# Optimization experiments

Hardware: AMD Instinct MI355X
Metric: run time of the kernel (lower is better)

## Reference

```python
import jax, jax.numpy as jnp
import numpy as np

EMBED_DIM = 1024
NUM_HEADS = 16
HEAD_DIM = EMBED_DIM // NUM_HEADS
BSZ = 4
SEQ = 1500


def setup_inputs() -> dict:
    key = jax.random.key(0)
    ks = jax.random.split(key, 8)
    s = 0.02
    return {
        "hidden_states": jax.random.normal(ks[0], (BSZ, SEQ, EMBED_DIM), jnp.float32),
        "Wq": jax.random.normal(ks[1], (EMBED_DIM, EMBED_DIM), jnp.float32) * s,
        "bq": jax.random.normal(ks[2], (EMBED_DIM,), jnp.float32) * s,
        "Wk": jax.random.normal(ks[3], (EMBED_DIM, EMBED_DIM), jnp.float32) * s,
        "Wv": jax.random.normal(ks[4], (EMBED_DIM, EMBED_DIM), jnp.float32) * s,
        "bv": jax.random.normal(ks[5], (EMBED_DIM,), jnp.float32) * s,
        "Wo": jax.random.normal(ks[6], (EMBED_DIM, EMBED_DIM), jnp.float32) * s,
        "bo": jax.random.normal(ks[7], (EMBED_DIM,), jnp.float32) * s,
    }


def reference(hidden_states, Wq, bq, Wk, Wv, bv, Wo, bo):
    b, t, e = hidden_states.shape
    h, d = NUM_HEADS, HEAD_DIM
    scaling = d ** -0.5

    def shape(x):  # [b, t, e] -> [b, h, t, d]
        return x.reshape(b, t, h, d).transpose(0, 2, 1, 3)

    # q_proj (with bias) then scale applied to the full projected output,
    # matching the original (scale multiplies q_proj output incl. bias).
    q = shape((hidden_states @ Wq.T + bq) * scaling)
    k = shape(hidden_states @ Wk.T)            # k_proj has no bias in Whisper
    v = shape(hidden_states @ Wv.T + bv)

    # naive materialized attention scores: [b, h, t, t]
    attn_weights = jnp.einsum("bhqd,bhkd->bhqk", q, k)
    attn_probs = jax.nn.softmax(attn_weights, axis=-1)
    attn_output = jnp.einsum("bhqk,bhkd->bhqd", attn_probs, v)

    # [b, h, t, d] -> [b, t, e]
    attn_output = attn_output.transpose(0, 2, 1, 3).reshape(b, t, e)
    return attn_output @ Wo.T + bo
```

## Files before the change

### kernel.cpp

```cpp
#include <hip/hip_runtime.h>
#include <math.h>

#define E 1024
#define NH 16
#define HD 64
#define BSZ_ 4
#define SEQ_ 1500
#define M_ (BSZ_ * SEQ_)
#define SZE ((size_t)M_ * (size_t)E)
#define QSC (0.125f * 1.44269504f)

#define QA_OFF  0u
#define XB_OFF  6144000u
#define WB_OFF  12288000u
#define WOB_OFF 15433728u
#define WS_NEED_BYTES ((size_t)(16482304u) * 2u)

typedef __attribute__((ext_vector_type(8))) short short8v;
typedef __attribute__((ext_vector_type(4))) float f32x4;
typedef __attribute__((ext_vector_type(16))) float f32x16;
typedef __attribute__((ext_vector_type(4))) unsigned short ushort4v;

__device__ __forceinline__ unsigned short f2bf(float f) {
    union { float f; unsigned int i; } c; c.f = f;
    return (unsigned short)((c.i + 0x7FFFu + ((c.i >> 16) & 1u)) >> 16);
}
__device__ __forceinline__ unsigned int cvt_pk_bf16(float a, float b) {
    unsigned int r;
    asm("v_cvt_pk_bf16_f32 %0, %1, %2" : "=v"(r) : "v"(a), "v"(b));
    return r;
}

__device__ __forceinline__ int swz(int row, int col) {
    return (row << 6) + ((((col >> 3) ^ row) & 7) << 3) + (col & 7);
}
__device__ __forceinline__ int swzf(int r, int d) {
    int row = r >> 1;
    int cs = ((r & 1) << 3) | (d >> 3);
    return row * 128 + ((cs ^ (row & 15)) << 3) + (d & 7);
}

__device__ __forceinline__ short8v pack8(const float* x) {
    union { unsigned int u[4]; short8v v; } r;
    r.u[0] = cvt_pk_bf16(x[0], x[1]);
    r.u[1] = cvt_pk_bf16(x[2], x[3]);
    r.u[2] = cvt_pk_bf16(x[4], x[5]);
    r.u[3] = cvt_pk_bf16(x[6], x[7]);
    return r.v;
}

__device__ __forceinline__ void gload16(const unsigned short* g,
                                        unsigned short* l) {
    __builtin_amdgcn_global_load_lds(
        (const __attribute__((address_space(1))) unsigned int*)(g),
        (__attribute__((address_space(3))) unsigned int*)(l), 16, 0, 0);
}


__global__ __launch_bounds__(256) void cvt_kernel(
    const float* __restrict__ X,  const float* __restrict__ Wk,
    const float* __restrict__ Wv, const float* __restrict__ Wq,
    const float* __restrict__ Wo, unsigned short* __restrict__ ws)
{
    size_t w = ((size_t)blockIdx.x * 256 + threadIdx.x) * 8;
    const float* s; unsigned short* d; float sc = 1.0f;
    if (w < 6144000u)      { s = X  + w;             d = ws + XB_OFF + w; }
    else if (w < 7192576u) { s = Wk + (w - 6144000u); d = ws + WB_OFF + (w - 6144000u); }
    else if (w < 8241152u) { s = Wv + (w - 7192576u); d = ws + WB_OFF + 1048576u + (w - 7192576u); }
    else if (w < 9289728u) { s = Wq + (w - 8241152u); d = ws + WB_OFF + 2097152u + (w - 8241152u); sc = QSC; }
    else                   { s = Wo + (w - 9289728u); d = ws + WOB_OFF + (w - 9289728u); }
    float t[8];
    *(float4*)t = *(const float4*)s;
    *(float4*)(t + 4) = *(const float4*)(s + 4);
#pragma unroll
    for (int i = 0; i < 8; ++i) t[i] *= sc;
    *(short8v*)d = pack8(t);
}

__device__ __forceinline__ void gemm128b(
    const unsigned short* __restrict__ Arow,
    const unsigned short* __restrict__ Brow,
    unsigned short* As, unsigned short* Bs, int tid, f32x4 acc[4][4])
{
    const int lane = tid & 63, wid = tid >> 6;
    const int wm = tid >> 7, wn = (tid >> 6) & 1;
    for (int k0 = 0; k0 < E; k0 += 64) {
#pragma unroll
        for (int i = 0; i < 4; ++i) {
            int row = wid * 32 + i * 8 + (lane >> 3);
            int sl = (lane & 7) ^ (row & 7);
            unsigned short* lbase = As + (wid * 32 + i * 8) * 64;
            gload16(Arow + (size_t)row * E + k0 + sl * 8, lbase);
            unsigned short* lbase2 = Bs + (wid * 32 + i * 8) * 64;
            gload16(Brow + (size_t)row * E + k0 + sl * 8, lbase2);
        }
        __syncthreads();
#pragma unroll
        for (int kk = 0; kk < 64; kk += 32) {
            short8v afr[4], bfr[4];
#pragma unroll
            for (int m = 0; m < 4; ++m)
                afr[m] = *(const short8v*)(As + swz(wm * 64 + m * 16 + (lane & 15),
                                                    kk + (lane >> 4) * 8));
#pragma unroll
            for (int n = 0; n < 4; ++n)
                bfr[n] = *(const short8v*)(Bs + swz(wn * 64 + n * 16 + (lane & 15),
                                                    kk + (lane >> 4) * 8));
            __builtin_amdgcn_s_setprio(1);
#pragma unroll
            for (int m = 0; m < 4; ++m)
#pragma unroll
                for (int n = 0; n < 4; ++n)
                    acc[m][n] = __builtin_amdgcn_mfma_f32_16x16x32_bf16(
                        afr[m], bfr[n], acc[m][n], 0, 0, 0);
            __builtin_amdgcn_s_setprio(0);
        }
        __syncthreads();
    }
}

__global__ __launch_bounds__(256) void proj_fast(
    const unsigned short* __restrict__ Xb, const unsigned short* __restrict__ Wb,
    const float* __restrict__ bv, const float* __restrict__ bq,
    unsigned short* __restrict__ Kb, unsigned short* __restrict__ Vt,
    unsigned short* __restrict__ Qa)
{
    __shared__ unsigned short As[128 * 64], Bs[128 * 64];
    const int sid = blockIdx.x;
    const int nid = (sid & 7) * 141 + (sid >> 3);
    const int mb = nid / 24, nb = nid % 24;
    const int z = nb >> 3;
    const size_t m0 = (size_t)mb * 128;
    const int tid = threadIdx.x, lane = tid & 63;
    const int wm = tid >> 7, wn = (tid >> 6) & 1;

    f32x4 acc[4][4];
#pragma unroll
    for (int m = 0; m < 4; ++m)
#pragma unroll
        for (int n = 0; n < 4; ++n)
#pragma unroll
            for (int i = 0; i < 4; ++i) acc[m][n][i] = 0.f;

    gemm128b(Xb + m0 * E, Wb + (size_t)nb * 128 * E, As, Bs, tid, acc);

#pragma unroll
    for (int m = 0; m < 4; ++m) {
        long gi0 = (long)m0 + wm * 64 + m * 16 + (lane >> 4) * 4;
#pragma unroll
        for (int n = 0; n < 4; ++n) {
            int col = (nb & 7) * 128 + wn * 64 + n * 16 + (lane & 15);
            if (z == 0) {
#pragma unroll
                for (int rg = 0; rg < 4; ++rg) {
                    long gi = gi0 + rg;
                    if (gi < M_) Kb[(size_t)gi * E + col] = f2bf(acc[m][n][rg]);
                }
            } else if (z == 2) {
                float bias = bq[col] * QSC;
#pragma unroll
                for (int rg = 0; rg < 4; ++rg) {
                    long gi = gi0 + rg;
                    if (gi < M_)
                        Qa[(size_t)gi * E + col] = f2bf(acc[m][n][rg] + bias);
                }
            } else {
                float bias = bv[col];
                if (gi0 + 3 < M_) {
                    long bb = gi0 / SEQ_, t0 = gi0 % SEQ_;
                    union { unsigned int u[2]; ushort4v v; } pk;
                    pk.u[0] = cvt_pk_bf16(acc[m][n][0] + bias, acc[m][n][1] + bias);
                    pk.u[1] = cvt_pk_bf16(acc[m][n][2] + bias, acc[m][n][3] + bias);
                    *(ushort4v*)(Vt + ((size_t)bb * E + col) * SEQ_ + t0) = pk.v;
                } else {
#pragma unroll
                    for (int rg = 0; rg < 4; ++rg) {
                        long gi = gi0 + rg;
                        if (gi < M_) {
                            long bb = gi / SEQ_, t = gi % SEQ_;
                            Vt[((size_t)bb * E + col) * SEQ_ + t] =
                                f2bf(acc[m][n][rg] + bias);
                        }
                    }
                }
            }
        }
    }
}

__global__ __launch_bounds__(256) void oproj_fast(
    const unsigned short* __restrict__ Ab, const unsigned short* __restrict__ Wob,
    const float* __restrict__ bo, float* __restrict__ out)
{
    __shared__ unsigned short As[128 * 64], Bs[128 * 64];
    const int sid = blockIdx.x;
    const int nid = (sid & 7) * 47 + (sid >> 3);
    const int mb = nid >> 3, nb = nid & 7;
    const size_t m0 = (size_t)mb * 128;
    const int tid = threadIdx.x, lane = tid & 63;
    const int wm = tid >> 7, wn = (tid >> 6) & 1;

    f32x4 acc[4][4];
#pragma unroll
    for (int m = 0; m < 4; ++m)
#pragma unroll
        for (int n = 0; n < 4; ++n)
#pragma unroll
            for (int i = 0; i < 4; ++i) acc[m][n][i] = 0.f;

    gemm128b(Ab + m0 * E, Wob + (size_t)nb * 128 * E, As, Bs, tid, acc);

#pragma unroll
    for (int m = 0; m < 4; ++m) {
        long gi0 = (long)m0 + wm * 64 + m * 16 + (lane >> 4) * 4;
#pragma unroll
        for (int n = 0; n < 4; ++n) {
            int col = nb * 128 + wn * 64 + n * 16 + (lane & 15);
            float bias = bo[col];
#pragma unroll
            for (int rg = 0; rg < 4; ++rg) {
                long gi = gi0 + rg;
                if (gi < M_) out[(size_t)gi * E + col] = acc[m][n][rg] + bias;
            }
        }
    }
}

template <bool ABF>
__device__ __forceinline__ void gemm128(
    const float* __restrict__ Af, const unsigned short* __restrict__ Ab,
    size_t arow0, int avalid,
    const float* __restrict__ W, int wrow0,
    unsigned short* As, unsigned short* Bs,
    int tid, f32x4 acc[4][4])
{
    const int lane = tid & 63;
    const int wm = (tid >> 7), wn = (tid >> 6) & 1;
    float4 pA[8]; short8v pAb[4]; float4 pB[8];

    auto loadT = [&](int k0) {
#pragma unroll
        for (int uu = 0; uu < 4; ++uu) {
            int u = tid + uu * 256, row = u >> 3, sl = (u & 7) * 8;
            if constexpr (ABF) {
                short8v t;
#pragma unroll
                for (int i = 0; i < 8; ++i) t[i] = 0;
                if (row < avalid)
                    t = *(const short8v*)(Ab + (arow0 + row) * E + k0 + sl);
                pAb[uu] = t;
            } else {
                float4 x0 = make_float4(0.f, 0.f, 0.f, 0.f), x1 = x0;
                if (row < avalid) {
                    const float* p = Af + (arow0 + row) * (size_t)E + k0 + sl;
                    x0 = *(const float4*)p; x1 = *(const float4*)(p + 4);
                }
                pA[2 * uu] = x0; pA[2 * uu + 1] = x1;
            }
            const float* q = W + (size_t)(wrow0 + row) * E + k0 + sl;
            pB[2 * uu] = *(const float4*)q;
            pB[2 * uu + 1] = *(const float4*)(q + 4);
        }
    };
    auto commitT = [&]() {
#pragma unroll
        for (int uu = 0; uu < 4; ++uu) {
            int u = tid + uu * 256, row = u >> 3, sl = (u & 7) * 8;
            if constexpr (ABF) {
                *(short8v*)(As + swz(row, sl)) = pAb[uu];
            } else {
                float t[8];
                *(float4*)t = pA[2 * uu]; *(float4*)(t + 4) = pA[2 * uu + 1];
                *(short8v*)(As + swz(row, sl)) = pack8(t);
            }
            float t2[8];
            *(float4*)t2 = pB[2 * uu]; *(float4*)(t2 + 4) = pB[2 * uu + 1];
            *(short8v*)(Bs + swz(row, sl)) = pack8(t2);
        }
    };

    loadT(0);
    for (int k0 = 0; k0 < E; k0 += 64) {
        __syncthreads();
        commitT();
        __syncthreads();
        if (k0 + 64 < E) loadT(k0 + 64);
#pragma unroll
        for (int kk = 0; kk < 64; kk += 32) {
            short8v afr[4], bfr[4];
#pragma unroll
            for (int m = 0; m < 4; ++m)
                afr[m] = *(const short8v*)(As + swz(wm * 64 + m * 16 + (lane & 15),
                                                    kk + (lane >> 4) * 8));
#pragma unroll
            for (int n = 0; n < 4; ++n)
                bfr[n] = *(const short8v*)(Bs + swz(wn * 64 + n * 16 + (lane & 15),
                                                    kk + (lane >> 4) * 8));
            __builtin_amdgcn_s_setprio(1);
#pragma unroll
            for (int m = 0; m < 4; ++m)
#pragma unroll
                for (int n = 0; n < 4; ++n)
                    acc[m][n] = __builtin_amdgcn_mfma_f32_16x16x32_bf16(
                        afr[m], bfr[n], acc[m][n], 0, 0, 0);
            __builtin_amdgcn_s_setprio(0);
        }
    }
}

__global__ __launch_bounds__(256, 2) void proj_kernel(
    const float* __restrict__ X, const float* __restrict__ Wk,
    const float* __restrict__ Wv, const float* __restrict__ bv,
    const float* __restrict__ Wq, const float* __restrict__ bq,
    unsigned short* __restrict__ Kb, unsigned short* __restrict__ Vt,
    unsigned short* __restrict__ Qo)
{
    __shared__ unsigned short As[128 * 64], Bs[128 * 64];
    const int sid = blockIdx.x, cpx = gridDim.x >> 3;
    const int nid = (sid & 7) * cpx + (sid >> 3);
    const int mb = nid / 24, nb = nid % 24;
    const int z = nb >> 3, nbz = nb & 7;
    const size_t m0 = (size_t)mb * 128;
    const int avalid = (M_ - (int)m0) < 128 ? (M_ - (int)m0) : 128;
    const float* W = (z == 0) ? Wk : (z == 1) ? Wv : Wq;

    f32x4 acc[4][4];
#pragma unroll
    for (int m = 0; m < 4; ++m)
#pragma unroll
        for (int n = 0; n < 4; ++n)
#pragma unroll
            for (int i = 0; i < 4; ++i) acc[m][n][i] = 0.f;

    gemm128<false>(X, nullptr, m0, avalid, W, nbz * 128, As, Bs, threadIdx.x, acc);

    const int tid = threadIdx.x, lane = tid & 63;
    const int wm = (tid >> 7), wn = (tid >> 6) & 1;
#pragma unroll
    for (int m = 0; m < 4; ++m) {
        long gi0 = (long)m0 + wm * 64 + m * 16 + (lane >> 4) * 4;
#pragma unroll
        for (int n = 0; n < 4; ++n) {
            int col = nbz * 128 + wn * 64 + n * 16 + (lane & 15);
            if (z == 0) {
#pragma unroll
                for (int rg = 0; rg < 4; ++rg) {
                    long gi = gi0 + rg;
                    if (gi < M_) Kb[(size_t)gi * E + col] = f2bf(acc[m][n][rg]);
                }
            } else if (z == 2) {
                float bias = bq[col];
#pragma unroll
                for (int rg = 0; rg < 4; ++rg) {
                    long gi = gi0 + rg;
                    if (gi < M_)
                        Qo[(size_t)gi * E + col] = f2bf((acc[m][n][rg] + bias) * QSC);
                }
            } else {
                float bias = bv[col];
                if (gi0 + 3 < M_) {
                    long bb = gi0 / SEQ_, t0 = gi0 % SEQ_;
                    union { unsigned int u[2]; ushort4v v; } pk;
                    pk.u[0] = cvt_pk_bf16(acc[m][n][0] + bias, acc[m][n][1] + bias);
                    pk.u[1] = cvt_pk_bf16(acc[m][n][2] + bias, acc[m][n][3] + bias);
                    *(ushort4v*)(Vt + ((size_t)bb * E + col) * SEQ_ + t0) = pk.v;
                } else {
#pragma unroll
                    for (int rg = 0; rg < 4; ++rg) {
                        long gi = gi0 + rg;
                        if (gi < M_) {
                            long bb = gi / SEQ_, t = gi % SEQ_;
                            Vt[((size_t)bb * E + col) * SEQ_ + t] =
                                f2bf(acc[m][n][rg] + bias);
                        }
                    }
                }
            }
        }
    }
}

__global__ __launch_bounds__(256, 2) void oproj_kernel(
    const unsigned short* __restrict__ Ab, const float* __restrict__ Wo,
    const float* __restrict__ bo, float* __restrict__ out)
{
    __shared__ unsigned short As[128 * 64], Bs[128 * 64];
    const int sid = blockIdx.x, cpx = gridDim.x >> 3;
    const int nid = (sid & 7) * cpx + (sid >> 3);
    const int mb = nid >> 3, nb = nid & 7;
    const size_t m0 = (size_t)mb * 128;
    const int avalid = (M_ - (int)m0) < 128 ? (M_ - (int)m0) : 128;

    f32x4 acc[4][4];
#pragma unroll
    for (int m = 0; m < 4; ++m)
#pragma unroll
        for (int n = 0; n < 4; ++n)
#pragma unroll
            for (int i = 0; i < 4; ++i) acc[m][n][i] = 0.f;

    gemm128<true>(nullptr, Ab, m0, avalid, Wo, nb * 128, As, Bs, threadIdx.x, acc);

    const int tid = threadIdx.x, lane = tid & 63;
    const int wm = (tid >> 7), wn = (tid >> 6) & 1;
#pragma unroll
    for (int m = 0; m < 4; ++m) {
        long gi0 = (long)m0 + wm * 64 + m * 16 + (lane >> 4) * 4;
#pragma unroll
        for (int n = 0; n < 4; ++n) {
            int col = nb * 128 + wn * 64 + n * 16 + (lane & 15);
            float bias = bo[col];
#pragma unroll
            for (int rg = 0; rg < 4; ++rg) {
                long gi = gi0 + rg;
                if (gi < M_) out[(size_t)gi * E + col] = acc[m][n][rg] + bias;
            }
        }
    }
}

__global__ __launch_bounds__(256, 3) void attn_kernel(
    const unsigned short* __restrict__ Kb,
    const unsigned short* __restrict__ Vt,
    unsigned short* __restrict__ Qa)
{
    __shared__ unsigned short ks[32 * 128], vs[32 * 128];
    const int sid = blockIdx.x;
    const int nid = (sid & 7) * 96 + (sid >> 3);
    const int bh = nid / 12, qb = nid % 12;
    const int b = bh >> 4, hh = bh & 15;
    const int tid = threadIdx.x, lane = tid & 63, wz = tid >> 6;
    const int c = lane & 31, g2 = lane >> 5;
    const int q0 = qb * 128 + wz * 32;

    const unsigned short* kbase = Kb + (size_t)b * SEQ_ * E + hh * 64;
    const unsigned short* vbase = Vt + ((size_t)b * E + hh * 64) * SEQ_;

    short8v kreg[2];
    ushort4v vreg[4];
    auto loadK = [&](int kt0) {
#pragma unroll
        for (int uu = 0; uu < 2; ++uu) {
            int u = tid + uu * 256, key = u >> 3, slot = (u & 7) * 8;
            short8v t;
#pragma unroll
            for (int i = 0; i < 8; ++i) t[i] = 0;
            int gk = kt0 + key;
            if (gk < SEQ_) t = *(const short8v*)(kbase + (size_t)gk * E + slot);
            kreg[uu] = t;
        }
    };
    auto loadV = [&](int kt0) {
#pragma unroll
        for (int uu = 0; uu < 4; ++uu) {
            int u = tid + uu * 256, d = u >> 4, q4 = (u & 15) * 4;
            ushort4v t; t[0] = t[1] = t[2] = t[3] = 0;
            int col = kt0 + q4, rem = SEQ_ - col;
            const unsigned short* src = vbase + (size_t)d * SEQ_ + col;
            if (rem >= 4) t = *(const ushort4v*)src;
            else { for (int e2 = 0; e2 < 4; ++e2) if (e2 < rem) t[e2] = src[e2]; }
            vreg[uu] = t;
        }
    };

    loadK(0); loadV(0);

    short8v qf[4];
    {
        int qr = q0 + c;
        bool ok = qr < SEQ_;
        const unsigned short* qp = Qa + ((size_t)b * SEQ_ + qr) * E + hh * 64 + 8 * g2;
#pragma unroll
        for (int t = 0; t < 4; ++t) {
            short8v zv;
#pragma unroll
            for (int i = 0; i < 8; ++i) zv[i] = 0;
            if (ok) zv = *(const short8v*)(qp + t * 16);
            qf[t] = zv;
        }
    }

    f32x16 o0, o1;
#pragma unroll
    for (int i = 0; i < 16; ++i) { o0[i] = 0.f; o1[i] = 0.f; }
    float lsum = 0.f;

    for (int kt0 = 0; kt0 < SEQ_; kt0 += 64) {
        __syncthreads();
#pragma unroll
        for (int uu = 0; uu < 2; ++uu) {
            int u = tid + uu * 256;
            *(short8v*)(ks + swzf(u >> 3, (u & 7) * 8)) = kreg[uu];
        }
#pragma unroll
        for (int uu = 0; uu < 4; ++uu) {
            int u = tid + uu * 256;
            *(ushort4v*)(vs + swzf(u >> 4, (u & 15) * 4)) = vreg[uu];
        }
        __syncthreads();
        if (kt0 + 64 < SEQ_) { loadK(kt0 + 64); loadV(kt0 + 64); }
        const bool tail = (kt0 + 64 > SEQ_);

#pragma unroll
        for (int nt = 0; nt < 2; ++nt) {
            f32x16 s;
#pragma unroll
            for (int i = 0; i < 16; ++i) s[i] = 0.f;
            __builtin_amdgcn_s_setprio(1);
#pragma unroll
            for (int t = 0; t < 4; ++t) {
                short8v af = *(const short8v*)(ks + swzf(nt * 32 + c, t * 16 + 8 * g2));
                s = __builtin_amdgcn_mfma_f32_32x32x16_bf16(af, qf[t], s, 0, 0, 0);
            }
            __builtin_amdgcn_s_setprio(0);
            if (tail) {
#pragma unroll
                for (int r = 0; r < 16; ++r) {
                    int key = kt0 + nt * 32 + (r & 3) + 8 * (r >> 2) + 4 * g2;
                    if (key >= SEQ_) s[r] = -1e30f;
                }
            }
            float p[16];
#pragma unroll
            for (int r = 0; r < 16; ++r) p[r] = exp2f(s[r]);
            float ls = 0.f;
#pragma unroll
            for (int r = 0; r < 16; ++r) ls += p[r];
            lsum += ls;
            unsigned int pk[8], sw[8];
#pragma unroll
            for (int h = 0; h < 8; ++h) pk[h] = cvt_pk_bf16(p[2 * h], p[2 * h + 1]);
#pragma unroll
            for (int h = 0; h < 8; ++h) sw[h] = __shfl_xor(pk[h], 32, 64);
            __builtin_amdgcn_s_setprio(1);
#pragma unroll
            for (int tau = 0; tau < 2; ++tau) {
                union { unsigned int w[4]; short8v v; } pa;
                pa.w[0] = g2 ? sw[4 * tau + 2] : pk[4 * tau + 0];
                pa.w[1] = g2 ? sw[4 * tau + 3] : pk[4 * tau + 1];
                pa.w[2] = g2 ? pk[4 * tau + 2] : sw[4 * tau + 0];
                pa.w[3] = g2 ? pk[4 * tau + 3] : sw[4 * tau + 1];
                int t = nt * 2 + tau;
                short8v vb0 = *(const short8v*)(vs + swzf(0 + c, t * 16 + 8 * g2));
                short8v vb1 = *(const short8v*)(vs + swzf(32 + c, t * 16 + 8 * g2));
                o0 = __builtin_amdgcn_mfma_f32_32x32x16_bf16(pa.v, vb0, o0, 0, 0, 0);
                o1 = __builtin_amdgcn_mfma_f32_32x32x16_bf16(pa.v, vb1, o1, 0, 0, 0);
            }
            __builtin_amdgcn_s_setprio(0);
        }
    }

    lsum += __shfl_xor(lsum, 32, 64);
    __syncthreads();
    float* lf = (float*)ks + wz * 32;
    if (lane < 32) lf[c] = 1.0f / lsum;
#pragma unroll
    for (int r = 0; r < 16; ++r) {
        int ql = (r & 3) + 8 * (r >> 2) + 4 * g2;
        int tq = q0 + ql;
        if (tq < SEQ_) {
            float inv = lf[ql];
            unsigned short* op = Qa + ((size_t)b * SEQ_ + tq) * E + hh * 64;
            op[c] = f2bf(o0[r] * inv);
            op[32 + c] = f2bf(o1[r] * inv);
        }
    }
}

extern "C" void kernel_launch(void* const* d_in, const int* in_sizes, int n_in,
                              void* d_out, int out_size, void* d_ws, size_t ws_size,
                              hipStream_t stream) {
    const float* hs = (const float*)d_in[0];
    const float* Wq = (const float*)d_in[1];
    const float* bq = (const float*)d_in[2];
    const float* Wk = (const float*)d_in[3];
    const float* Wv = (const float*)d_in[4];
    const float* bv = (const float*)d_in[5];
    const float* Wo = (const float*)d_in[6];
    const float* bo = (const float*)d_in[7];

    unsigned short* Kb = (unsigned short*)d_out;
    unsigned short* Vt = (unsigned short*)d_out + SZE;
    unsigned short* ws = (unsigned short*)d_ws;
    unsigned short* Qa = ws + QA_OFF;
    float* out = (float*)d_out;

    if (ws_size >= WS_NEED_BYTES) {
        cvt_kernel<<<dim3(5048), 256, 0, stream>>>(hs, Wk, Wv, Wq, Wo, ws);
        proj_fast<<<dim3(1128), 256, 0, stream>>>(ws + XB_OFF, ws + WB_OFF,
                                                  bv, bq, Kb, Vt, Qa);
        attn_kernel<<<dim3(768), 256, 0, stream>>>(Kb, Vt, Qa);
        oproj_fast<<<dim3(376), 256, 0, stream>>>(Qa, ws + WOB_OFF, bo, out);
    } else {
        proj_kernel<<<dim3(47 * 24), 256, 0, stream>>>(hs, Wk, Wv, bv, Wq, bq,
                                                       Kb, Vt, Qa);
        attn_kernel<<<dim3(768), 256, 0, stream>>>(Kb, Vt, Qa);
        oproj_kernel<<<dim3(47 * 8), 256, 0, stream>>>(Qa, Wo, bo, out);
    }
}
```

Measured before the change: 179.8 us.

## Double-buffer K/V LDS tiles and swap shuffles for permlane32 in attention

The attention kernel now ping-pongs between two LDS buffers for K and V, so each tile is committed to shared memory after the current tile's compute. This removes one of the two barriers per iteration. The softmax exponentials use the raw hardware exp2 builtin with split partial sums, and the cross-half exchange of packed probabilities uses v_permlane32_swap in place of eight ds-based shuffles. Occupancy hint is raised from 3 to 4 blocks per CU, at the cost of doubled LDS per block and tighter register limits, which may cause spills.

```diff
diff --git a/kernel.cpp b/kernel.cpp
--- a/kernel.cpp
+++ b/kernel.cpp
@@ -29,6 +29,9 @@
     unsigned int r;
     asm("v_cvt_pk_bf16_f32 %0, %1, %2" : "=v"(r) : "v"(a), "v"(b));
     return r;
+}
+__device__ __forceinline__ void perml32(unsigned int &a, unsigned int &b) {
+    asm("v_permlane32_swap_b32 %0, %1" : "+v"(a), "+v"(b));
 }
 
 __device__ __forceinline__ int swz(int row, int col) {
@@ -419,12 +422,12 @@
     }
 }
 
-__global__ __launch_bounds__(256, 3) void attn_kernel(
+__global__ __launch_bounds__(256, 4) void attn_kernel(
     const unsigned short* __restrict__ Kb,
     const unsigned short* __restrict__ Vt,
     unsigned short* __restrict__ Qa)
 {
-    __shared__ unsigned short ks[32 * 128], vs[32 * 128];
+    __shared__ unsigned short ks[2][32 * 128], vs[2][32 * 128];
     const int sid = blockIdx.x;
     const int nid = (sid & 7) * 96 + (sid >> 3);
     const int bh = nid / 12, qb = nid % 12;
@@ -462,6 +465,18 @@
             vreg[uu] = t;
         }
     };
+    auto commitKV = [&](unsigned short* kd, unsigned short* vd) {
+#pragma unroll
+        for (int uu = 0; uu < 2; ++uu) {
+            int u = tid + uu * 256;
+            *(short8v*)(kd + swzf(u >> 3, (u & 7) * 8)) = kreg[uu];
+        }
+#pragma unroll
+        for (int uu = 0; uu < 4; ++uu) {
+            int u = tid + uu * 256;
+            *(ushort4v*)(vd + swzf(u >> 4, (u & 15) * 4)) = vreg[uu];
+        }
+    };
 
     loadK(0); loadV(0);
 
@@ -485,20 +500,15 @@
     for (int i = 0; i < 16; ++i) { o0[i] = 0.f; o1[i] = 0.f; }
     float lsum = 0.f;
 
-    for (int kt0 = 0; kt0 < SEQ_; kt0 += 64) {
-        __syncthreads();
-#pragma unroll
-        for (int uu = 0; uu < 2; ++uu) {
-            int u = tid + uu * 256;
-            *(short8v*)(ks + swzf(u >> 3, (u & 7) * 8)) = kreg[uu];
-        }
-#pragma unroll
-        for (int uu = 0; uu < 4; ++uu) {
-            int u = tid + uu * 256;
-            *(ushort4v*)(vs + swzf(u >> 4, (u & 15) * 4)) = vreg[uu];
-        }
-        __syncthreads();
-        if (kt0 + 64 < SEQ_) { loadK(kt0 + 64); loadV(kt0 + 64); }
+    commitKV(ks[0], vs[0]);
+    __syncthreads();
+    loadK(64); loadV(64);
+
+    const int NT = (SEQ_ + 63) / 64;
+    for (int it = 0; it < NT; ++it) {
+        const int kt0 = it * 64;
+        const unsigned short* kcur = ks[it & 1];
+        const unsigned short* vcur = vs[it & 1];
         const bool tail = (kt0 + 64 > SEQ_);
 
 #pragma unroll
@@ -509,7 +519,7 @@
             __builtin_amdgcn_s_setprio(1);
 #pragma unroll
             for (int t = 0; t < 4; ++t) {
-                short8v af = *(const short8v*)(ks + swzf(nt * 32 + c, t * 16 + 8 * g2));
+                short8v af = *(const short8v*)(kcur + swzf(nt * 32 + c, t * 16 + 8 * g2));
                 s = __builtin_amdgcn_mfma_f32_32x32x16_bf16(af, qf[t], s, 0, 0, 0);
             }
             __builtin_amdgcn_s_setprio(0);
@@ -520,39 +530,45 @@
                     if (key >= SEQ_) s[r] = -1e30f;
                 }
             }
-            float p[16];
-#pragma unroll
-            for (int r = 0; r < 16; ++r) p[r] = exp2f(s[r]);
-            float ls = 0.f;
-#pragma unroll
-            for (int r = 0; r < 16; ++r) ls += p[r];
-            lsum += ls;
-            unsigned int pk[8], sw[8];
-#pragma unroll
-            for (int h = 0; h < 8; ++h) pk[h] = cvt_pk_bf16(p[2 * h], p[2 * h + 1]);
-#pragma unroll
-            for (int h = 0; h < 8; ++h) sw[h] = __shfl_xor(pk[h], 32, 64);
+            unsigned int pk[8];
+            float ls0 = 0.f, ls1 = 0.f;
+#pragma unroll
+            for (int h = 0; h < 8; ++h) {
+                float p0 = __builtin_amdgcn_exp2f(s[2 * h]);
+                float p1 = __builtin_amdgcn_exp2f(s[2 * h + 1]);
+                if (h & 1) ls1 += p0 + p1; else ls0 += p0 + p1;
+                pk[h] = cvt_pk_bf16(p0, p1);
+            }
+            lsum += ls0 + ls1;
+            perml32(pk[0], pk[2]); perml32(pk[1], pk[3]);
+            perml32(pk[4], pk[6]); perml32(pk[5], pk[7]);
             __builtin_amdgcn_s_setprio(1);
 #pragma unroll
             for (int tau = 0; tau < 2; ++tau) {
                 union { unsigned int w[4]; short8v v; } pa;
-                pa.w[0] = g2 ? sw[4 * tau + 2] : pk[4 * tau + 0];
-                pa.w[1] = g2 ? sw[4 * tau + 3] : pk[4 * tau + 1];
-                pa.w[2] = g2 ? pk[4 * tau + 2] : sw[4 * tau + 0];
-                pa.w[3] = g2 ? pk[4 * tau + 3] : sw[4 * tau + 1];
+                pa.w[0] = pk[4 * tau + 0];
+                pa.w[1] = pk[4 * tau + 1];
+                pa.w[2] = pk[4 * tau + 2];
+                pa.w[3] = pk[4 * tau + 3];
                 int t = nt * 2 + tau;
-                short8v vb0 = *(const short8v*)(vs + swzf(0 + c, t * 16 + 8 * g2));
-                short8v vb1 = *(const short8v*)(vs + swzf(32 + c, t * 16 + 8 * g2));
+                short8v vb0 = *(const short8v*)(vcur + swzf(0 + c, t * 16 + 8 * g2));
+                short8v vb1 = *(const short8v*)(vcur + swzf(32 + c, t * 16 + 8 * g2));
                 o0 = __builtin_amdgcn_mfma_f32_32x32x16_bf16(pa.v, vb0, o0, 0, 0, 0);
                 o1 = __builtin_amdgcn_mfma_f32_32x32x16_bf16(pa.v, vb1, o1, 0, 0, 0);
             }
             __builtin_amdgcn_s_setprio(0);
         }
+
+        if (it + 1 < NT) {
+            commitKV(ks[(it + 1) & 1], vs[(it + 1) & 1]);
+            __syncthreads();
+            if (it + 2 < NT) { loadK(kt0 + 128); loadV(kt0 + 128); }
+        }
     }
 
     lsum += __shfl_xor(lsum, 32, 64);
     __syncthreads();
-    float* lf = (float*)ks + wz * 32;
+    float* lf = (float*)ks[0] + wz * 32;
     if (lane < 32) lf[c] = 1.0f / lsum;
 #pragma unroll
     for (int r = 0; r < 16; ++r) {
```

After: 182.3 us. About the same (+1.4%).
